# Kernel optimization log

Measured on AMD Instinct MI355X. Metric: run time of the kernel, lower is better.

Reference implementation:

```python
import jax, jax.numpy as jnp
import numpy as np

INPUT_DIM = 512
EMBED_DIM = 64
B, S = 4, 4096


def setup_inputs() -> dict:
    key = jax.random.key(0)
    ks = jax.random.split(key, 9)
    scale = 1.0 / np.sqrt(INPUT_DIM)
    return {
        "q": jax.random.normal(ks[0], (B, S, INPUT_DIM), dtype=jnp.float32),
        "k": jax.random.normal(ks[1], (B, S, INPUT_DIM), dtype=jnp.float32),
        "v": jax.random.normal(ks[2], (B, S, INPUT_DIM), dtype=jnp.float32),
        "Wq": jax.random.uniform(ks[3], (INPUT_DIM, EMBED_DIM), jnp.float32, -scale, scale),
        "bq": jax.random.uniform(ks[4], (EMBED_DIM,), jnp.float32, -scale, scale),
        "Wk": jax.random.uniform(ks[5], (INPUT_DIM, EMBED_DIM), jnp.float32, -scale, scale),
        "bk": jax.random.uniform(ks[6], (EMBED_DIM,), jnp.float32, -scale, scale),
        "Wv": jax.random.uniform(ks[7], (INPUT_DIM, EMBED_DIM), jnp.float32, -scale, scale),
        "bv": jax.random.uniform(ks[8], (EMBED_DIM,), jnp.float32, -scale, scale),
    }


def reference(q, k, v, Wq, bq, Wk, bk, Wv, bv):
    # Linear projections (torch Linear: x @ W^T + b; here W stored as [in, out])
    Q = q @ Wq + bq  # [B, S, E]
    K = k @ Wk + bk  # [B, S, E]
    V = v @ Wv + bv  # [B, S, E]
    d_k = K.shape[-1]
    scores = jnp.einsum("bqe,bke->bqk", Q, K) / jnp.sqrt(jnp.float32(d_k))  # [B, S, S]
    attn = jax.nn.softmax(scores, axis=-1)
    return jnp.einsum("bqk,bke->bqe", attn, V)  # [B, S, E]
```

## Files before the change

### kernel.cpp

```cpp
#include <hip/hip_runtime.h>
#include <math.h>

#define S_ 4096
#define C_SCALE 0.18033688011112042f
#define KSPLIT 8

typedef __attribute__((ext_vector_type(4))) float  floatx4;
typedef __attribute__((ext_vector_type(4))) short  short4_t;
typedef __attribute__((ext_vector_type(8))) short  short8_t;
typedef __attribute__((ext_vector_type(2))) unsigned int uintx2;
typedef __attribute__((ext_vector_type(4))) unsigned int uintx4;

__device__ __forceinline__ short f2bf(float f) {
  unsigned u = __builtin_bit_cast(unsigned, f);
  u += 0x7FFFu + ((u >> 16) & 1u);
  return (short)(u >> 16);
}
__device__ __forceinline__ unsigned pack2(float lo, float hi) {
  unsigned a = __builtin_bit_cast(unsigned, lo) + 0x8000u;
  unsigned b = __builtin_bit_cast(unsigned, hi) + 0x8000u;
  return __builtin_amdgcn_perm(b, a, 0x07060302u);
}
__device__ __forceinline__ unsigned packt(float lo, float hi) {
  return __builtin_amdgcn_perm(__builtin_bit_cast(unsigned, hi),
                               __builtin_bit_cast(unsigned, lo), 0x07060302u);
}
__device__ __forceinline__ float bf2f(short s) {
  return __builtin_bit_cast(float, (unsigned)((unsigned short)s) << 16);
}
__device__ __forceinline__ void dma16(const void* g, void* l) {
  __builtin_amdgcn_global_load_lds(
      (const __attribute__((address_space(1))) void*)g,
      (__attribute__((address_space(3))) void*)l, 16, 0, 0);
}

__global__ __launch_bounds__(256) void prep_w(const float* __restrict__ Wq,
                                              const float* __restrict__ Wk,
                                              const float* __restrict__ Wv,
                                              short* __restrict__ Wt) {
  __shared__ float T[64 * 65];
  int m = blockIdx.x >> 3, kt = blockIdx.x & 7, tid = threadIdx.x;
  const float* W = (m == 0) ? Wq : (m == 1) ? Wk : Wv;
  float sc = (m == 0) ? C_SCALE : 1.0f;
#pragma unroll
  for (int i = 0; i < 16; i++) {
    int e = i * 256 + tid;
    int k = e >> 6, n = e & 63;
    T[k * 65 + n] = W[(kt * 64 + k) * 64 + n];
  }
  __syncthreads();
#pragma unroll
  for (int i = 0; i < 16; i++) {
    int e = i * 256 + tid;
    int n = e >> 6, k = e & 63;
    Wt[m * 32768 + n * 512 + kt * 64 + k] = f2bf(T[k * 65 + n] * sc);
  }
}

__global__ __launch_bounds__(256, 3) void proj_kernel(
    const float* __restrict__ qin, const float* __restrict__ kin,
    const float* __restrict__ vin, const float* __restrict__ bq,
    const float* __restrict__ bk, const float* __restrict__ bv,
    const short* __restrict__ Wt, short* __restrict__ Qp,
    short* __restrict__ Kp, short* __restrict__ Vt) {
  __shared__ short A_lds[64 * 64];
  __shared__ short W_lds[64 * 64];

  int tid = threadIdx.x;
  int m = blockIdx.x >> 8;
  int r0 = (blockIdx.x & 255) * 64;
  int wid = tid >> 6, lane = tid & 63, l15 = lane & 15, quad = lane >> 4;

  const float* in = (m == 0) ? qin : (m == 1) ? kin : vin;
  const short* Wm = Wt + m * 32768;

  int sr = tid >> 3, sc = tid & 7;
  int sphys = ((sc ^ (sr & 7)) * 8);

  floatx4 ar[4];
  auto loadA = [&](int kc) {
    const float* p = in + (size_t)(r0 + sr) * 512 + kc * 64 + sc * 8;
    ar[0] = *(const floatx4*)p;
    ar[1] = *(const floatx4*)(p + 4);
    const float* p2 = p + 32 * 512;
    ar[2] = *(const floatx4*)p2;
    ar[3] = *(const floatx4*)(p2 + 4);
  };
  auto dmaW = [&](int kc) {
#pragma unroll
    for (int j = 0; j < 2; j++) {
      int slot = wid * 128 + j * 64 + lane;
      int r = slot >> 3, c = slot & 7;
      int gc = (c ^ (r & 7)) * 8;
      dma16(Wm + r * 512 + kc * 64 + gc, (void*)&W_lds[(wid * 2 + j) * 512]);
    }
  };

  floatx4 acc[4];
#pragma unroll
  for (int nb = 0; nb < 4; nb++) acc[nb] = (floatx4){0.f, 0.f, 0.f, 0.f};

  loadA(0);
#pragma unroll
  for (int kc = 0; kc < 8; kc++) {
    if (kc) __syncthreads();
    dmaW(kc);
    uintx4 w0 = {pack2(ar[0][0], ar[0][1]), pack2(ar[0][2], ar[0][3]),
                 pack2(ar[1][0], ar[1][1]), pack2(ar[1][2], ar[1][3])};
    uintx4 w1 = {pack2(ar[2][0], ar[2][1]), pack2(ar[2][2], ar[2][3]),
                 pack2(ar[3][0], ar[3][1]), pack2(ar[3][2], ar[3][3])};
    *(short8_t*)(A_lds + sr * 64 + sphys) = __builtin_bit_cast(short8_t, w0);
    *(short8_t*)(A_lds + (sr + 32) * 64 + sphys) = __builtin_bit_cast(short8_t, w1);
    if (kc < 7) loadA(kc + 1);
    __syncthreads();
    int arow = wid * 16 + l15;
    int akey = arow & 7, wkey = l15 & 7;
#pragma unroll
    for (int h = 0; h < 2; h++) {
      short8_t af = *(const short8_t*)(A_lds + arow * 64 + ((h * 4 + quad) ^ akey) * 8);
#pragma unroll
      for (int nb = 0; nb < 4; nb++) {
        short8_t wf = *(const short8_t*)(W_lds + (nb * 16 + l15) * 64 +
                                         ((h * 4 + quad) ^ wkey) * 8);
        acc[nb] = __builtin_amdgcn_mfma_f32_16x16x32_bf16(af, wf, acc[nb], 0, 0, 0);
      }
    }
  }

  const float* bias = (m == 0) ? bq : (m == 1) ? bk : bv;
  float bsc = (m == 0) ? C_SCALE : 1.0f;
  if (m < 2) {
    short* out = (m == 0) ? Qp : Kp;
#pragma unroll
    for (int nb = 0; nb < 4; nb++) {
      float bv_ = bias[nb * 16 + l15] * bsc;
#pragma unroll
      for (int r = 0; r < 4; r++)
        out[(size_t)(r0 + wid * 16 + quad * 4 + r) * 64 + nb * 16 + l15] =
            f2bf(acc[nb][r] + bv_);
    }
  } else {
    int bb = r0 >> 12;
    int s0 = (r0 & 4095) + wid * 16 + quad * 4;
#pragma unroll
    for (int nb = 0; nb < 4; nb++) {
      float bv_ = bias[nb * 16 + l15];
      short4_t pk = {f2bf(acc[nb][0] + bv_), f2bf(acc[nb][1] + bv_),
                     f2bf(acc[nb][2] + bv_), f2bf(acc[nb][3] + bv_)};
      *(short4_t*)(Vt + (size_t)bb * 262144 + (nb * 16 + l15) * 4096 + s0) = pk;
    }
  }
}

__global__ __launch_bounds__(256, 2) void attn_kernel(
    const short* __restrict__ Qp, const short* __restrict__ Kp,
    const short* __restrict__ Vt, short* __restrict__ Po,
    float* __restrict__ Lp) {
  __shared__ short K_lds[2][64 * 64];
  __shared__ short V_lds[2][64 * 64];
  __shared__ short P_lds[4][64 * 64];

  int tid = threadIdx.x;
  int ks = blockIdx.x >> 6, b = (blockIdx.x >> 4) & 3, qt = blockIdx.x & 15;
  int wid = tid >> 6, lane = tid & 63, l15 = lane & 15, quad = lane >> 4;
  int key = l15 & 7;

  const short* Qb = Qp + (size_t)b * (S_ * 64);
  const short* Kb = Kp + (size_t)b * (S_ * 64);
  const short* Vb = Vt + (size_t)b * (64 * S_);

  int q0 = qt * 256 + wid * 64;

  short8_t qf[4][2];
#pragma unroll
  for (int qs = 0; qs < 4; qs++)
#pragma unroll
    for (int h = 0; h < 2; h++)
      qf[qs][h] = *(const short8_t*)(Qb + (q0 + qs * 16 + l15) * 64 + h * 32 + quad * 8);

  floatx4 o[4][4];
#pragma unroll
  for (int qs = 0; qs < 4; qs++)
#pragma unroll
    for (int eb = 0; eb < 4; eb++) o[qs][eb] = (floatx4){0.f, 0.f, 0.f, 0.f};
  float l_acc[4] = {0.f, 0.f, 0.f, 0.f};
  short* Pw = &P_lds[wid][0];
  int ks_base = ks * 512;

  auto stage = [&](int t, int buf) {
    int ks0 = ks_base + t * 64;
#pragma unroll
    for (int j = 0; j < 2; j++) {
      int slot = wid * 128 + j * 64 + lane;
      int r = slot >> 3, c = slot & 7;
      int gc = (c ^ (r & 7)) * 8;
      dma16(Kb + (ks0 + r) * 64 + gc, (void*)&K_lds[buf][(wid * 2 + j) * 512]);
      dma16(Vb + (size_t)r * 4096 + ks0 + gc, (void*)&V_lds[buf][(wid * 2 + j) * 512]);
    }
  };

  stage(0, 0);
  for (int t = 0; t < 8; t++) {
    __syncthreads();
    if (t < 7) stage(t + 1, (t + 1) & 1);
    __syncthreads();
    const short* Kt = K_lds[t & 1];
    const short* Vl = V_lds[t & 1];

#pragma unroll
    for (int jh = 0; jh < 2; jh++) {
      short8_t kA[4];
#pragma unroll
      for (int jb = 0; jb < 2; jb++)
#pragma unroll
        for (int eh = 0; eh < 2; eh++)
          kA[jb * 2 + eh] = *(const short8_t*)(
              Kt + (jh * 32 + jb * 16 + l15) * 64 + ((eh * 4 + quad) ^ key) * 8);

#pragma unroll
      for (int qs = 0; qs < 4; qs++) {
        floatx4 z = (floatx4){0.f, 0.f, 0.f, 0.f};
        floatx4 s0 = __builtin_amdgcn_mfma_f32_16x16x32_bf16(kA[0], qf[qs][0], z, 0, 0, 0);
        s0 = __builtin_amdgcn_mfma_f32_16x16x32_bf16(kA[1], qf[qs][1], s0, 0, 0, 0);
        floatx4 s1 = __builtin_amdgcn_mfma_f32_16x16x32_bf16(kA[2], qf[qs][0], z, 0, 0, 0);
        s1 = __builtin_amdgcn_mfma_f32_16x16x32_bf16(kA[3], qf[qs][1], s1, 0, 0, 0);
        float e00 = __builtin_amdgcn_exp2f(s0[0]), e01 = __builtin_amdgcn_exp2f(s0[1]);
        float e02 = __builtin_amdgcn_exp2f(s0[2]), e03 = __builtin_amdgcn_exp2f(s0[3]);
        float e10 = __builtin_amdgcn_exp2f(s1[0]), e11 = __builtin_amdgcn_exp2f(s1[1]);
        float e12 = __builtin_amdgcn_exp2f(s1[2]), e13 = __builtin_amdgcn_exp2f(s1[3]);
        l_acc[qs] += ((e00 + e01) + (e02 + e03)) + ((e10 + e11) + (e12 + e13));
        int row = (qs * 16 + l15) * 64;
        uintx2 w0 = {packt(e00, e01), packt(e02, e03)};
        uintx2 w1 = {packt(e10, e11), packt(e12, e13)};
        *(uintx2*)(Pw + row + ((jh * 4 + 0 + (quad >> 1)) ^ key) * 8 + (quad & 1) * 4) = w0;
        *(uintx2*)(Pw + row + ((jh * 4 + 2 + (quad >> 1)) ^ key) * 8 + (quad & 1) * 4) = w1;
      }

      short8_t pf[4];
#pragma unroll
      for (int qs = 0; qs < 4; qs++)
        pf[qs] = *(const short8_t*)(Pw + (qs * 16 + l15) * 64 +
                                    ((jh * 4 + quad) ^ key) * 8);
#pragma unroll
      for (int eb = 0; eb < 4; eb++) {
        short8_t vf = *(const short8_t*)(Vl + (eb * 16 + l15) * 64 +
                                         ((jh * 4 + quad) ^ key) * 8);
#pragma unroll
        for (int qs = 0; qs < 4; qs++)
          o[qs][eb] = __builtin_amdgcn_mfma_f32_16x16x32_bf16(pf[qs], vf, o[qs][eb], 0, 0, 0);
      }
    }
  }

#pragma unroll
  for (int qs = 0; qs < 4; qs++) {
    float l = l_acc[qs];
    l += __shfl_xor(l, 16, 64);
    l += __shfl_xor(l, 32, 64);
    int grow_base = b * 4096 + q0 + qs * 16;
    short* Pb = Po + ((size_t)ks * 16384 + grow_base) * 64;
#pragma unroll
    for (int eb = 0; eb < 4; eb++)
#pragma unroll
      for (int r = 0; r < 4; r++)
        Pb[(size_t)(quad * 4 + r) * 64 + eb * 16 + l15] = f2bf(o[qs][eb][r]);
    if (quad == 0) Lp[ks * 16384 + grow_base + l15] = l;
  }
}

__global__ __launch_bounds__(256) void combine_kernel(
    const short* __restrict__ Po, const float* __restrict__ Lp,
    float* __restrict__ out) {
  int gid = blockIdx.x * 256 + threadIdx.x;
  int grow = gid >> 3, e0 = (gid & 7) * 8;
  float s[8];
#pragma unroll
  for (int i = 0; i < 8; i++) s[i] = 0.f;
  float l = 0.f;
#pragma unroll
  for (int ks = 0; ks < KSPLIT; ks++) {
    short8_t p = *(const short8_t*)(Po + ((size_t)ks * 16384 + grow) * 64 + e0);
#pragma unroll
    for (int i = 0; i < 8; i++) s[i] += bf2f(p[i]);
    l += Lp[ks * 16384 + grow];
  }
  float inv = 1.0f / l;
  floatx4 o0 = {s[0] * inv, s[1] * inv, s[2] * inv, s[3] * inv};
  floatx4 o1 = {s[4] * inv, s[5] * inv, s[6] * inv, s[7] * inv};
  *(floatx4*)(out + (size_t)grow * 64 + e0) = o0;
  *(floatx4*)(out + (size_t)grow * 64 + e0 + 4) = o1;
}

extern "C" void kernel_launch(void* const* d_in, const int* in_sizes, int n_in,
                              void* d_out, int out_size, void* d_ws, size_t ws_size,
                              hipStream_t stream) {
  const float* q = (const float*)d_in[0];
  const float* k = (const float*)d_in[1];
  const float* v = (const float*)d_in[2];
  const float* Wq = (const float*)d_in[3];
  const float* bq = (const float*)d_in[4];
  const float* Wk = (const float*)d_in[5];
  const float* bk = (const float*)d_in[6];
  const float* Wv = (const float*)d_in[7];
  const float* bv = (const float*)d_in[8];

  char* ws = (char*)d_ws;
  short* Qp = (short*)(ws);
  short* Kp = (short*)(ws + (1u << 21));
  short* Vt = (short*)(ws + (2u << 21));
  short* Wt = (short*)(ws + (3u << 21));
  short* Po = (short*)(ws + (4u << 21));
  float* Lp = (float*)(ws + (13u << 21));

  prep_w<<<24, 256, 0, stream>>>(Wq, Wk, Wv, Wt);
  proj_kernel<<<768, 256, 0, stream>>>(q, k, v, bq, bk, bv, Wt, Qp, Kp, Vt);
  attn_kernel<<<512, 256, 0, stream>>>(Qp, Kp, Vt, Po, Lp);
  combine_kernel<<<512, 256, 0, stream>>>(Po, Lp, (float*)d_out);
}
```

Measured before the change: 164.4 us.

## Double-buffer projection LDS tiles, drop redundant attention barrier, raise PV MFMA priority

The projection kernel now keeps two LDS buffers for the A and W tiles and two register sets for the A prefetch. The W DMA for step kc+1 and the global load of A for step kc+2 are issued right after the barrier, so they overlap the current MFMA work, and each step needs only one barrier. In the attention kernel, the second barrier after staging the next K/V tile is removed, since the top barrier already covers both the read-after-write and write-after-read hazards. The P·V MFMA block is wrapped in s_setprio so this wave gets issue priority there. The cost is double the LDS footprint in the projection kernel, which may reduce occupancy, and barrier correctness now depends on the implicit vmcnt wait before each barrier.

```diff
diff --git a/kernel.cpp b/kernel.cpp
--- a/kernel.cpp
+++ b/kernel.cpp
@@ -63,8 +63,8 @@
     const float* __restrict__ bk, const float* __restrict__ bv,
     const short* __restrict__ Wt, short* __restrict__ Qp,
     short* __restrict__ Kp, short* __restrict__ Vt) {
-  __shared__ short A_lds[64 * 64];
-  __shared__ short W_lds[64 * 64];
+  __shared__ short A_lds[2][64 * 64];
+  __shared__ short W_lds[2][64 * 64];
 
   int tid = threadIdx.x;
   int m = blockIdx.x >> 8;
@@ -77,51 +77,56 @@
   int sr = tid >> 3, sc = tid & 7;
   int sphys = ((sc ^ (sr & 7)) * 8);
 
-  floatx4 ar[4];
-  auto loadA = [&](int kc) {
-    const float* p = in + (size_t)(r0 + sr) * 512 + kc * 64 + sc * 8;
-    ar[0] = *(const floatx4*)p;
-    ar[1] = *(const floatx4*)(p + 4);
-    const float* p2 = p + 32 * 512;
-    ar[2] = *(const floatx4*)p2;
-    ar[3] = *(const floatx4*)(p2 + 4);
+  floatx4 ar[2][4];
+  auto loadA = [&](int kc, int p) {
+    const float* pA = in + (size_t)(r0 + sr) * 512 + kc * 64 + sc * 8;
+    ar[p][0] = *(const floatx4*)pA;
+    ar[p][1] = *(const floatx4*)(pA + 4);
+    const float* p2 = pA + 32 * 512;
+    ar[p][2] = *(const floatx4*)p2;
+    ar[p][3] = *(const floatx4*)(p2 + 4);
   };
-  auto dmaW = [&](int kc) {
+  auto dmaW = [&](int kc, int buf) {
 #pragma unroll
     for (int j = 0; j < 2; j++) {
       int slot = wid * 128 + j * 64 + lane;
       int r = slot >> 3, c = slot & 7;
       int gc = (c ^ (r & 7)) * 8;
-      dma16(Wm + r * 512 + kc * 64 + gc, (void*)&W_lds[(wid * 2 + j) * 512]);
+      dma16(Wm + r * 512 + kc * 64 + gc, (void*)&W_lds[buf][(wid * 2 + j) * 512]);
     }
   };
+  auto packStoreA = [&](int p, int buf) {
+    uintx4 w0 = {pack2(ar[p][0][0], ar[p][0][1]), pack2(ar[p][0][2], ar[p][0][3]),
+                 pack2(ar[p][1][0], ar[p][1][1]), pack2(ar[p][1][2], ar[p][1][3])};
+    uintx4 w1 = {pack2(ar[p][2][0], ar[p][2][1]), pack2(ar[p][2][2], ar[p][2][3]),
+                 pack2(ar[p][3][0], ar[p][3][1]), pack2(ar[p][3][2], ar[p][3][3])};
+    *(short8_t*)(&A_lds[buf][sr * 64 + sphys]) = __builtin_bit_cast(short8_t, w0);
+    *(short8_t*)(&A_lds[buf][(sr + 32) * 64 + sphys]) = __builtin_bit_cast(short8_t, w1);
+  };
 
   floatx4 acc[4];
 #pragma unroll
   for (int nb = 0; nb < 4; nb++) acc[nb] = (floatx4){0.f, 0.f, 0.f, 0.f};
 
-  loadA(0);
+  loadA(0, 0);
+  loadA(1, 1);
+  dmaW(0, 0);
 #pragma unroll
   for (int kc = 0; kc < 8; kc++) {
-    if (kc) __syncthreads();
-    dmaW(kc);
-    uintx4 w0 = {pack2(ar[0][0], ar[0][1]), pack2(ar[0][2], ar[0][3]),
-                 pack2(ar[1][0], ar[1][1]), pack2(ar[1][2], ar[1][3])};
-    uintx4 w1 = {pack2(ar[2][0], ar[2][1]), pack2(ar[2][2], ar[2][3]),
-                 pack2(ar[3][0], ar[3][1]), pack2(ar[3][2], ar[3][3])};
-    *(short8_t*)(A_lds + sr * 64 + sphys) = __builtin_bit_cast(short8_t, w0);
-    *(short8_t*)(A_lds + (sr + 32) * 64 + sphys) = __builtin_bit_cast(short8_t, w1);
-    if (kc < 7) loadA(kc + 1);
+    packStoreA(kc & 1, kc & 1);
     __syncthreads();
+    if (kc < 7) dmaW(kc + 1, (kc + 1) & 1);
+    if (kc < 6) loadA(kc + 2, kc & 1);
     int arow = wid * 16 + l15;
     int akey = arow & 7, wkey = l15 & 7;
 #pragma unroll
     for (int h = 0; h < 2; h++) {
-      short8_t af = *(const short8_t*)(A_lds + arow * 64 + ((h * 4 + quad) ^ akey) * 8);
+      short8_t af =
+          *(const short8_t*)(&A_lds[kc & 1][arow * 64 + ((h * 4 + quad) ^ akey) * 8]);
 #pragma unroll
       for (int nb = 0; nb < 4; nb++) {
-        short8_t wf = *(const short8_t*)(W_lds + (nb * 16 + l15) * 64 +
-                                         ((h * 4 + quad) ^ wkey) * 8);
+        short8_t wf = *(const short8_t*)(&W_lds[kc & 1][(nb * 16 + l15) * 64 +
+                                                        ((h * 4 + quad) ^ wkey) * 8]);
         acc[nb] = __builtin_amdgcn_mfma_f32_16x16x32_bf16(af, wf, acc[nb], 0, 0, 0);
       }
     }
@@ -203,7 +208,6 @@
   for (int t = 0; t < 8; t++) {
     __syncthreads();
     if (t < 7) stage(t + 1, (t + 1) & 1);
-    __syncthreads();
     const short* Kt = K_lds[t & 1];
     const short* Vl = V_lds[t & 1];
 
@@ -241,6 +245,7 @@
       for (int qs = 0; qs < 4; qs++)
         pf[qs] = *(const short8_t*)(Pw + (qs * 16 + l15) * 64 +
                                     ((jh * 4 + quad) ^ key) * 8);
+      __builtin_amdgcn_s_setprio(1);
 #pragma unroll
       for (int eb = 0; eb < 4; eb++) {
         short8_t vf = *(const short8_t*)(Vl + (eb * 16 + l15) * 64 +
@@ -249,6 +254,7 @@
         for (int qs = 0; qs < 4; qs++)
           o[qs][eb] = __builtin_amdgcn_mfma_f32_16x16x32_bf16(pf[qs], vf, o[qs][eb], 0, 0, 0);
       }
+      __builtin_amdgcn_s_setprio(0);
     }
   }
 
```

Result: no change. 165.2 us, median of 2 (+0.5%).
